# Kernel optimization log

Hardware: AMD Instinct MI355X
Metric: run time of the kernel (lower is better)

## Reference

```python
import jax, jax.numpy as jnp
import numpy as np

NEG_SLOPE = 0.2  # DGL GATConv/GATv2Conv default negative_slope


def _seg_softmax(score, dst, N):
    # softmax over incoming edges per destination node; score: (E, H)
    m = jax.ops.segment_max(score, dst, num_segments=N)          # (N, H)
    ex = jnp.exp(score - m[dst])
    s = jax.ops.segment_sum(ex, dst, num_segments=N)             # (N, H)
    return ex / s[dst]


def _gatv2(h, src, dst, Ws, Wd, attn, bias, N):
    # GATv2: e_ij = a^T LeakyReLU(W_s h_src + W_d h_dst)
    H, D = attn.shape
    fs = (h @ Ws).reshape(N, H, D)
    fd = (h @ Wd).reshape(N, H, D)
    e = jax.nn.leaky_relu(fs[src] + fd[dst], NEG_SLOPE)          # (E, H, D)
    score = jnp.einsum('ehd,hd->eh', e, attn)                    # (E, H)
    alpha = _seg_softmax(score, dst, N)
    out = jax.ops.segment_sum(fs[src] * alpha[:, :, None], dst, num_segments=N)
    return out + bias.reshape(1, H, D)                           # (N, H, D)


def _gat(h, src, dst, W, al, ar, bias, N):
    # GAT v1: e_ij = LeakyReLU(a_l . W h_src + a_r . W h_dst)
    H, D = al.shape
    f = (h @ W).reshape(N, H, D)
    el = jnp.einsum('nhd,hd->nh', f, al)
    er = jnp.einsum('nhd,hd->nh', f, ar)
    score = jax.nn.leaky_relu(el[src] + er[dst], NEG_SLOPE)      # (E, H)
    alpha = _seg_softmax(score, dst, N)
    out = jax.ops.segment_sum(f[src] * alpha[:, :, None], dst, num_segments=N)
    return out + bias.reshape(1, H, D)                           # (N, H, D)


def setup_inputs() -> dict:
    key = jax.random.key(0)
    N, E, V, ED = 50000, 800000, 32, 128   # nodes, edges, node types, embed_dim
    H, D = 4, 32                           # heads, per-head dim (hidden = 128)
    ks = jax.random.split(key, 20)
    rn = lambda k, shp, s: jax.random.normal(k, shp, dtype=jnp.float32) * s
    hid = H * D
    return {
        'in_feat': jax.random.randint(ks[0], (N,), 0, V),
        'src': jax.random.randint(ks[1], (E,), 0, N),
        'dst': jax.random.randint(ks[2], (E,), 0, N),
        'emb': rn(ks[3], (V, ED), 0.02),
        'W1s': rn(ks[4], (ED, hid), 1.0 / np.sqrt(ED)),
        'W1d': rn(ks[5], (ED, hid), 1.0 / np.sqrt(ED)),
        'a1': rn(ks[6], (H, D), 1.0 / np.sqrt(D)),
        'b1': jnp.zeros((hid,), jnp.float32),
        'W2s': rn(ks[7], (hid, hid), 1.0 / np.sqrt(hid)),
        'W2d': rn(ks[8], (hid, hid), 1.0 / np.sqrt(hid)),
        'a2': rn(ks[9], (H, D), 1.0 / np.sqrt(D)),
        'b2': jnp.zeros((hid,), jnp.float32),
        'Wc': rn(ks[10], (hid, H * V), 1.0 / np.sqrt(hid)),
        'al': rn(ks[11], (H, V), 1.0 / np.sqrt(V)),
        'ar': rn(ks[12], (H, V), 1.0 / np.sqrt(V)),
        'bc': jnp.zeros((H * V,), jnp.float32),
    }


def reference(in_feat, src, dst, emb, W1s, W1d, a1, b1, W2s, W2d, a2, b2, Wc, al, ar, bc):
    N = in_feat.shape[0]
    h = emb[in_feat]                                              # (N, 128)
    h = jax.nn.elu(_gatv2(h, src, dst, W1s, W1d, a1, b1, N).reshape(N, -1))
    h = jax.nn.elu(_gatv2(h, src, dst, W2s, W2d, a2, b2, N).reshape(N, -1))
    h = _gat(h, src, dst, Wc, al, ar, bc, N)                      # (N, H, V)
    return jax.nn.softmax(h.mean(axis=1), axis=-1)                # (N, V)
```

## Files before the change

### kernel.cpp

```cpp
#include <hip/hip_runtime.h>
#include <hip/hip_bf16.h>

typedef unsigned short u16;
typedef unsigned int u32;

typedef __bf16 bf16x8 __attribute__((ext_vector_type(8)));
typedef float f32x4 __attribute__((ext_vector_type(4)));

#define NEG_SLOPE 0.2f
#define CAP 5120

__device__ __forceinline__ float bf2f(u16 u){
  union { u32 i; float f; } c; c.i = ((u32)u) << 16; return c.f;
}
__device__ __forceinline__ u16 f2bf(float f){
  __hip_bfloat16 h = __float2bfloat16(f);
  u16 u; __builtin_memcpy(&u, &h, 2); return u;
}
__device__ __forceinline__ u32 pack2(float a, float b){
  return (u32)f2bf(a) | ((u32)f2bf(b) << 16);
}
__device__ __forceinline__ float2 bfpair(u32 v){
  union { u32 i; float f; } a, b;
  a.i = v << 16; b.i = v & 0xffff0000u;
  return make_float2(a.f, b.f);
}
__device__ __forceinline__ float lrelu(float x){
  return fmaxf(x, 0.f) + NEG_SLOPE * fminf(x, 0.f);
}
__device__ __forceinline__ float eluf(float x){
  return x > 0.f ? x : (__expf(x) - 1.f);
}
__device__ __forceinline__ bf16x8 ld_frag(const uint4* p){
  uint4 u = *p;
  bf16x8 r;
  __builtin_memcpy(&r, &u, 16);
  return r;
}

__global__ void k_probe(const u16* __restrict__ w, int* __restrict__ flag){
  int t = threadIdx.x;
  int hit = 0;
  for (int i = t; i < 4096; i += 64){
    u16 v = w[i];
    int e = (v >> 7) & 0xFF;
    if (e >= 200) hit = 1;
  }
  unsigned long long b = __ballot(hit);
  if (t == 0) flag[0] = b ? 1 : 0;
}

struct Params13 {
  const void* src[13];
  int off[13];
  int n[13];
};

__global__ void k_cvt(Params13 P, const int* __restrict__ flag, float* __restrict__ dst){
  int t = blockIdx.y;
  int i = blockIdx.x*256 + threadIdx.x;
  if (i >= P.n[t]) return;
  int f = flag[0];
  float v = f ? ((const float*)P.src[t])[i] : bf2f(((const u16*)P.src[t])[i]);
  dst[P.off[t] + i] = v;
}

__global__ void k_wprep(const float* __restrict__ pr, u16* __restrict__ wp){
  int g = blockIdx.x*256 + threadIdx.x;
  if (g >= 3*16384) return;
  int m = g >> 14;
  int e = g & 16383;
  int j    = e & 7;
  int lane = (e >> 3) & 63;
  int kb   = (e >> 9) & 3;
  int nt   = (e >> 11) & 7;
  int k = kb*32 + (lane >> 4)*8 + j;
  int n = nt*16 + (lane & 15);
  const int Woff[3] = {37120, 53504, 70144};
  wp[g] = f2bf(pr[Woff[m] + k*128 + n]);
}

__global__ void k_t1prep(const float* __restrict__ Ts, u16* __restrict__ tp){
  int g = blockIdx.x*256 + threadIdx.x;
  if (g >= 16384) return;
  int j    = g & 7;
  int lane = (g >> 3) & 63;
  int kb   = (g >> 9) & 3;
  int nt   = (g >> 11) & 7;
  int k = kb*32 + (lane >> 4)*8 + j;
  int n = nt*16 + (lane & 15);
  int h = k >> 5, hp = n >> 5, v = k & 31;
  tp[g] = (h == hp) ? f2bf(Ts[v*128 + n]) : (u16)0;
}

__global__ __launch_bounds__(256) void k_bin(
    const int* __restrict__ src, const int* __restrict__ dst, const int* __restrict__ vf,
    int* __restrict__ gcnt, u32* __restrict__ bbuf, int E){
  __shared__ int lcnt[256];
  __shared__ int lloc[256];
  int t = threadIdx.x;
  lcnt[t] = 0;
  __syncthreads();
  int base = blockIdx.x*2048;
  int s[8], d[8];
  #pragma unroll
  for (int k=0;k<8;++k){
    int i = base + k*256 + t;
    if (i < E){ s[k]=src[i]; d[k]=dst[i]; atomicAdd(&lcnt[d[k]>>8], 1); }
    else s[k] = -1;
  }
  __syncthreads();
  if (lcnt[t] > 0) lloc[t] = atomicAdd(&gcnt[t], lcnt[t]);
  __syncthreads();
  #pragma unroll
  for (int k=0;k<8;++k){
    if (s[k] >= 0){
      int b = d[k]>>8;
      int pos = atomicAdd(&lloc[b], 1);
      if (pos < CAP)
        bbuf[(size_t)b*CAP + pos] = ((u32)s[k]<<13) | ((u32)vf[s[k]]<<8) | (u32)(d[k]&255);
    }
  }
}

__global__ __launch_bounds__(256) void k_bcnt(
    const u32* __restrict__ bbuf, const int* __restrict__ gcnt,
    u32* __restrict__ H, int* __restrict__ deg, int N){
  __shared__ u32 lh[8192];
  __shared__ int ldeg[256];
  int b = blockIdx.x;
  int t = threadIdx.x;
  for (int i=t;i<8192;i+=256) lh[i]=0;
  ldeg[t]=0;
  __syncthreads();
  int n = gcnt[b]; if (n > CAP) n = CAP;
  const u32* bb = bbuf + (size_t)b*CAP;
  for (int i=t;i<n;i+=256){
    u32 it = bb[i];
    int ld = it & 255, v = (it>>8)&31;
    atomicAdd(&lh[ld*32+v], 1u);
    atomicAdd(&ldeg[ld], 1);
  }
  __syncthreads();
  int node0 = b*256;
  for (int i=t;i<8192;i+=256){
    int ld = i>>5;
    if (node0+ld < N) H[(size_t)(node0+ld)*32 + (i&31)] = lh[i];
  }
  if (node0+t < N) deg[node0+t] = ldeg[t];
}

__global__ __launch_bounds__(256) void k_csort(
    const u32* __restrict__ bbuf, const int* __restrict__ gcnt,
    const int* __restrict__ rowptr, int* __restrict__ esrc, int N){
  __shared__ int cur[256];
  int b = blockIdx.x;
  int t = threadIdx.x;
  int node0 = b*256;
  cur[t] = (node0+t < N) ? rowptr[node0+t] : 0;
  __syncthreads();
  int n = gcnt[b]; if (n > CAP) n = CAP;
  const u32* bb = bbuf + (size_t)b*CAP;
  for (int i=t;i<n;i+=256){
    u32 it = bb[i];
    int ld = it & 255;
    int pos = atomicAdd(&cur[ld], 1);
    esrc[pos] = (int)(it >> 13);
  }
}

__global__ __launch_bounds__(256) void k_bsum(const int* __restrict__ deg,
                                              int* __restrict__ bsum, int N){
  __shared__ int ws[4];
  int t = threadIdx.x;
  int i = blockIdx.x*256 + t;
  int v = (i < N) ? deg[i] : 0;
  #pragma unroll
  for (int off=32; off>=1; off>>=1) v += __shfl_down(v, off);
  if ((t & 63) == 0) ws[t>>6] = v;
  __syncthreads();
  if (t == 0) bsum[blockIdx.x] = ws[0]+ws[1]+ws[2]+ws[3];
}

__global__ void k_scanb(const int* __restrict__ bsum, int* __restrict__ boff,
                        int* __restrict__ rowptr, int nb, int N){
  int l = threadIdx.x;
  int carry = 0;
  int nChunk = (nb + 63) >> 6;
  for (int c = 0; c < nChunk; ++c){
    int idx = (c << 6) + l;
    int v = (idx < nb) ? bsum[idx] : 0;
    int x = v;
    #pragma unroll
    for (int off=1; off<64; off<<=1){
      int y = __shfl_up(x, off);
      if (l >= off) x += y;
    }
    if (idx < nb) boff[idx] = carry + x - v;
    carry += __shfl(x, 63);
  }
  if (l == 0) rowptr[N] = carry;
}

__global__ __launch_bounds__(256) void k_scan2(const int* __restrict__ deg,
                                               const int* __restrict__ boff,
                                               int* __restrict__ rowptr, int N){
  __shared__ int ws[4];
  int t = threadIdx.x;
  int i = blockIdx.x*256 + t;
  int lane = t & 63, wid = t >> 6;
  int v = (i < N) ? deg[i] : 0;
  int x = v;
  #pragma unroll
  for (int off=1; off<64; off<<=1){
    int y = __shfl_up(x, off);
    if (lane >= off) x += y;
  }
  if (lane == 63) ws[wid] = x;
  __syncthreads();
  int woff = 0;
  #pragma unroll
  for (int w=0; w<4; ++w) woff += (w < wid) ? ws[w] : 0;
  int excl = boff[blockIdx.x] + woff + x - v;
  if (i < N) rowptr[i] = excl;
}

__global__ void k_tinyA(const float* __restrict__ pr,
                        float* __restrict__ Ts, float* __restrict__ Td){
  const float* emb = pr + 0;
  const float* W1s = pr + 4096;
  const float* W1d = pr + 20480;
  int g = blockIdx.x*256 + threadIdx.x;
  int v = g >> 7, j = g & 127;
  float as = 0.f, ad = 0.f;
  for (int k = 0; k < 128; ++k){
    float e = emb[v*128 + k];
    as += e * W1s[k*128 + j];
    ad += e * W1d[k*128 + j];
  }
  Ts[g] = as; Td[g] = ad;
}

__global__ void k_tinyB(const float* __restrict__ Ts, const float* __restrict__ Td,
                        const float* __restrict__ pr, float* __restrict__ S1){
  const float* a1 = pr + 36864;
  int g = blockIdx.x*256 + threadIdx.x;
  int vd = g >> 7, vs = (g >> 2) & 31, h = g & 3;
  float acc = 0.f;
  for (int dd = 0; dd < 32; ++dd){
    float x = Ts[vs*128 + h*32 + dd] + Td[vd*128 + h*32 + dd];
    acc += a1[h*32 + dd] * lrelu(x);
  }
  S1[g] = acc;
}

__global__ void k_tinyC(const float* __restrict__ S1, float* __restrict__ Ee){
  int g = blockIdx.x*256 + threadIdx.x;
  int vd = g >> 7, h = g & 3;
  float M = -INFINITY;
  #pragma unroll 8
  for (int vs = 0; vs < 32; ++vs) M = fmaxf(M, S1[vd*128 + vs*4 + h]);
  Ee[g] = __expf(S1[g] - M);
}

__global__ __launch_bounds__(256) void k_node1w(
    const u32* __restrict__ H, const int* __restrict__ vf,
    const float* __restrict__ Ee, u16* __restrict__ wnb, int N){
  int t = threadIdx.x;
  int wid = t >> 6, lane = t & 63;
  int base = blockIdx.x * 32;
  for (int dd = wid; dd < 32; dd += 4){
    int d = base + dd;
    if (d >= N) break;
    int tt = vf[d];
    float4 w4 = make_float4(0.f,0.f,0.f,0.f);
    if (lane < 32){
      float cf = (float)H[(size_t)d*32 + lane];
      const float4 e4 = *reinterpret_cast<const float4*>(Ee + tt*128 + lane*4);
      w4.x = cf*e4.x; w4.y = cf*e4.y; w4.z = cf*e4.z; w4.w = cf*e4.w;
    }
    float4 sv = w4;
    #pragma unroll
    for (int off=1; off<32; off<<=1){
      sv.x += __shfl_xor(sv.x, off);
      sv.y += __shfl_xor(sv.y, off);
      sv.z += __shfl_xor(sv.z, off);
      sv.w += __shfl_xor(sv.w, off);
    }
    if (lane < 32){
      float ix = (sv.x > 0.f) ? 1.f/sv.x : 0.f;
      float iy = (sv.y > 0.f) ? 1.f/sv.y : 0.f;
      float iz = (sv.z > 0.f) ? 1.f/sv.z : 0.f;
      float iw = (sv.w > 0.f) ? 1.f/sv.w : 0.f;
      u16* row = wnb + (size_t)d*128;
      row[      lane] = f2bf(w4.x*ix);
      row[ 32 + lane] = f2bf(w4.y*iy);
      row[ 64 + lane] = f2bf(w4.z*iz);
      row[ 96 + lane] = f2bf(w4.w*iw);
    }
  }
}

template<bool TWO>
__global__ __launch_bounds__(256) void k_mfma(
    const u32* __restrict__ Xb, const u16* __restrict__ wpS, const u16* __restrict__ wpD,
    u16* __restrict__ outS, u16* __restrict__ outD, int N){
  int t = threadIdx.x;
  int w = t >> 6, l = t & 63;
  int row0 = blockIdx.x*64 + w*16;
  int ar = row0 + (l & 15);
  int ko = l >> 4;
  const uint4* Xq = reinterpret_cast<const uint4*>(Xb);
  bf16x8 a[4];
  #pragma unroll
  for (int kb=0;kb<4;++kb){
    if (ar < N) a[kb] = ld_frag(&Xq[(size_t)ar*16 + kb*4 + ko]);
    else { uint4 z = make_uint4(0,0,0,0); __builtin_memcpy(&a[kb], &z, 16); }
  }
  const uint4* WS = reinterpret_cast<const uint4*>(wpS);
  const uint4* WD = reinterpret_cast<const uint4*>(wpD);
  int col0 = l & 15;
  int rbase = row0 + (l>>4)*4;
  #pragma unroll
  for (int nt=0; nt<8; ++nt){
    f32x4 accS = {0.f,0.f,0.f,0.f};
    f32x4 accD = {0.f,0.f,0.f,0.f};
    #pragma unroll
    for (int kb=0;kb<4;++kb){
      bf16x8 bS = ld_frag(&WS[(nt*4 + kb)*64 + l]);
      accS = __builtin_amdgcn_mfma_f32_16x16x32_bf16(a[kb], bS, accS, 0,0,0);
      if (TWO){
        bf16x8 bD = ld_frag(&WD[(nt*4 + kb)*64 + l]);
        accD = __builtin_amdgcn_mfma_f32_16x16x32_bf16(a[kb], bD, accD, 0,0,0);
      }
    }
    int col = nt*16 + col0;
    #pragma unroll
    for (int r=0;r<4;++r){
      int rr = rbase + r;
      if (rr < N){
        outS[(size_t)rr*128 + col] = f2bf(accS[r]);
        if (TWO) outD[(size_t)rr*128 + col] = f2bf(accD[r]);
      }
    }
  }
}

__global__ __launch_bounds__(256) void k_mfma1(
    const u32* __restrict__ Xb, const u16* __restrict__ tp, const float* __restrict__ pr,
    u16* __restrict__ outB, int N){
  const float* b1 = pr + 36992;
  int t = threadIdx.x;
  int w = t >> 6, l = t & 63;
  int row0 = blockIdx.x*64 + w*16;
  int ar = row0 + (l & 15);
  int ko = l >> 4;
  const uint4* Xq = reinterpret_cast<const uint4*>(Xb);
  bf16x8 a[4];
  #pragma unroll
  for (int kb=0;kb<4;++kb){
    if (ar < N) a[kb] = ld_frag(&Xq[(size_t)ar*16 + kb*4 + ko]);
    else { uint4 z = make_uint4(0,0,0,0); __builtin_memcpy(&a[kb], &z, 16); }
  }
  const uint4* WB = reinterpret_cast<const uint4*>(tp);
  int col0 = l & 15;
  int rbase = row0 + (l>>4)*4;
  #pragma unroll
  for (int nt=0; nt<8; ++nt){
    f32x4 acc = {0.f,0.f,0.f,0.f};
    #pragma unroll
    for (int kb=0;kb<4;++kb){
      bf16x8 b = ld_frag(&WB[(nt*4 + kb)*64 + l]);
      acc = __builtin_amdgcn_mfma_f32_16x16x32_bf16(a[kb], b, acc, 0,0,0);
    }
    int col = nt*16 + col0;
    float bv = b1[col];
    #pragma unroll
    for (int r=0;r<4;++r){
      int rr = rbase + r;
      if (rr < N) outB[(size_t)rr*128 + col] = f2bf(eluf(acc[r] + bv));
    }
  }
}

#define UNPACK8(pv, fv)                                              \
  { float2 _p0 = bfpair(pv.x), _p1 = bfpair(pv.y),                   \
           _p2 = bfpair(pv.z), _p3 = bfpair(pv.w);                   \
    fv[0]=_p0.x; fv[1]=_p0.y; fv[2]=_p1.x; fv[3]=_p1.y;              \
    fv[4]=_p2.x; fv[5]=_p2.y; fv[6]=_p3.x; fv[7]=_p3.y; }

__global__ __launch_bounds__(256) void k_node2f(
    const int* __restrict__ rowptr, const int* __restrict__ esrc,
    const u32* __restrict__ fsb, const u32* __restrict__ fdb,
    const float* __restrict__ pr, u32* __restrict__ hOutB, int N){
  const float* a2 = pr + 69888;
  const float* b2 = pr + 70016;
  int t = threadIdx.x;
  int wid = t >> 6, lane = t & 63;
  int q = lane & 15, g = lane >> 4;
  int d = blockIdx.x*4 + wid;
  if (d >= N) return;
  int r0 = rowptr[d], r1 = rowptr[d+1];
  const uint4* fs4 = reinterpret_cast<const uint4*>(fsb);
  float a2r[8], fdr[8];
  {
    float4 t0 = *reinterpret_cast<const float4*>(a2 + q*8);
    float4 t1 = *reinterpret_cast<const float4*>(a2 + q*8 + 4);
    a2r[0]=t0.x; a2r[1]=t0.y; a2r[2]=t0.z; a2r[3]=t0.w;
    a2r[4]=t1.x; a2r[5]=t1.y; a2r[6]=t1.z; a2r[7]=t1.w;
    uint4 pv = reinterpret_cast<const uint4*>(fdb)[(size_t)d*16 + q];
    UNPACK8(pv, fdr);
  }
  float m = -INFINITY, ssum = 0.f;
  float acc[8] = {0.f,0.f,0.f,0.f,0.f,0.f,0.f,0.f};
  int i = r0 + g;
  for (; i + 4 < r1; i += 8){
    int s1 = esrc[i], s2 = esrc[i+4];
    uint4 pv1 = fs4[(size_t)s1*16 + q];
    uint4 pv2 = fs4[(size_t)s2*16 + q];
    float f1[8], f2[8];
    UNPACK8(pv1, f1);
    UNPACK8(pv2, f2);
    float p1a = 0.f, p1b = 0.f, p2a = 0.f, p2b = 0.f;
    #pragma unroll
    for (int k=0;k<8;++k){
      float x1 = f1[k] + fdr[k];
      float x2 = f2[k] + fdr[k];
      p1a = fmaf(a2r[k], x1, p1a);
      p1b = fmaf(a2r[k], fabsf(x1), p1b);
      p2a = fmaf(a2r[k], x2, p2a);
      p2b = fmaf(a2r[k], fabsf(x2), p2b);
    }
    float p1 = fmaf(0.6f, p1a, 0.4f*p1b);
    float p2 = fmaf(0.6f, p2a, 0.4f*p2b);
    p1 += __shfl_xor(p1, 1); p1 += __shfl_xor(p1, 2);
    p2 += __shfl_xor(p2, 1); p2 += __shfl_xor(p2, 2);
    float mn = fmaxf(m, fmaxf(p1, p2));
    float cor = __expf(m - mn);
    float w1 = __expf(p1 - mn);
    float w2 = __expf(p2 - mn);
    ssum = ssum*cor + w1 + w2;
    #pragma unroll
    for (int k=0;k<8;++k) acc[k] = fmaf(acc[k], cor, fmaf(w1, f1[k], w2*f2[k]));
    m = mn;
  }
  for (; i < r1; i += 4){
    int s = esrc[i];
    uint4 pv = fs4[(size_t)s*16 + q];
    float fv[8];
    UNPACK8(pv, fv);
    float pa = 0.f, pb = 0.f;
    #pragma unroll
    for (int k=0;k<8;++k){
      float x = fv[k] + fdr[k];
      pa = fmaf(a2r[k], x, pa);
      pb = fmaf(a2r[k], fabsf(x), pb);
    }
    float p = fmaf(0.6f, pa, 0.4f*pb);
    p += __shfl_xor(p, 1); p += __shfl_xor(p, 2);
    float mn = fmaxf(m, p);
    float cor = __expf(m - mn);
    float w = __expf(p - mn);
    ssum = ssum*cor + w;
    #pragma unroll
    for (int k=0;k<8;++k) acc[k] = fmaf(acc[k], cor, w*fv[k]);
    m = mn;
  }
  #pragma unroll
  for (int off = 16; off <= 32; off <<= 1){
    float mo  = __shfl_xor(m, off);
    float sso = __shfl_xor(ssum, off);
    float ao[8];
    #pragma unroll
    for (int k=0;k<8;++k) ao[k] = __shfl_xor(acc[k], off);
    float mn = fmaxf(m, mo);
    float c1 = (m  > -1e30f) ? __expf(m  - mn) : 0.f;
    float c2 = (mo > -1e30f) ? __expf(mo - mn) : 0.f;
    ssum = ssum*c1 + sso*c2;
    #pragma unroll
    for (int k=0;k<8;++k) acc[k] = acc[k]*c1 + ao[k]*c2;
    m = mn;
  }
  if (g == 0){
    float inv = (ssum > 0.f) ? 1.f/ssum : 0.f;
    float v0 = eluf(acc[0]*inv + b2[q*8+0]), v1 = eluf(acc[1]*inv + b2[q*8+1]);
    float v2 = eluf(acc[2]*inv + b2[q*8+2]), v3 = eluf(acc[3]*inv + b2[q*8+3]);
    float v4 = eluf(acc[4]*inv + b2[q*8+4]), v5 = eluf(acc[5]*inv + b2[q*8+5]);
    float v6 = eluf(acc[6]*inv + b2[q*8+6]), v7 = eluf(acc[7]*inv + b2[q*8+7]);
    uint4 ov;
    ov.x = pack2(v0,v1); ov.y = pack2(v2,v3);
    ov.z = pack2(v4,v5); ov.w = pack2(v6,v7);
    *reinterpret_cast<uint4*>(hOutB + (size_t)d*64 + q*4) = ov;
  }
}

__global__ __launch_bounds__(256) void k_node3f(
    const int* __restrict__ rowptr, const int* __restrict__ esrc,
    const float* __restrict__ el, const float* __restrict__ er, const u32* __restrict__ fb,
    const float* __restrict__ pr, const int* __restrict__ flag,
    void* __restrict__ out, int N){
  const float* bc = pr + 86784;
  int t = threadIdx.x;
  int wid = t >> 6, lane = t & 63;
  int q = lane & 15, g = lane >> 4;
  int h = q >> 2;
  int d = blockIdx.x*4 + wid;
  if (d >= N) return;
  int r0 = rowptr[d], r1 = rowptr[d+1];
  const uint4* f4g = reinterpret_cast<const uint4*>(fb);
  float erh = er[(size_t)d*4 + h];
  float m = -INFINITY, ssum = 0.f;
  float acc[8] = {0.f,0.f,0.f,0.f,0.f,0.f,0.f,0.f};
  int i = r0 + g;
  for (; i + 4 < r1; i += 8){
    int s1 = esrc[i], s2 = esrc[i+4];
    float sc1 = lrelu(el[(size_t)s1*4 + h] + erh);
    float sc2 = lrelu(el[(size_t)s2*4 + h] + erh);
    uint4 pv1 = f4g[(size_t)s1*16 + q];
    uint4 pv2 = f4g[(size_t)s2*16 + q];
    float f1[8], f2[8];
    UNPACK8(pv1, f1);
    UNPACK8(pv2, f2);
    float mn = fmaxf(m, fmaxf(sc1, sc2));
    float cor = __expf(m - mn);
    float w1 = __expf(sc1 - mn);
    float w2 = __expf(sc2 - mn);
    ssum = ssum*cor + w1 + w2;
    #pragma unroll
    for (int k=0;k<8;++k) acc[k] = fmaf(acc[k], cor, fmaf(w1, f1[k], w2*f2[k]));
    m = mn;
  }
  for (; i < r1; i += 4){
    int s = esrc[i];
    float sc = lrelu(el[(size_t)s*4 + h] + erh);
    uint4 pv = f4g[(size_t)s*16 + q];
    float fv[8];
    UNPACK8(pv, fv);
    float mn = fmaxf(m, sc);
    float cor = __expf(m - mn);
    float w = __expf(sc - mn);
    ssum = ssum*cor + w;
    #pragma unroll
    for (int k=0;k<8;++k) acc[k] = fmaf(acc[k], cor, w*fv[k]);
    m = mn;
  }
  #pragma unroll
  for (int off = 16; off <= 32; off <<= 1){
    float mo  = __shfl_xor(m, off);
    float sso = __shfl_xor(ssum, off);
    float ao[8];
    #pragma unroll
    for (int k=0;k<8;++k) ao[k] = __shfl_xor(acc[k], off);
    float mn = fmaxf(m, mo);
    float c1 = (m  > -1e30f) ? __expf(m  - mn) : 0.f;
    float c2 = (mo > -1e30f) ? __expf(mo - mn) : 0.f;
    ssum = ssum*c1 + sso*c2;
    #pragma unroll
    for (int k=0;k<8;++k) acc[k] = acc[k]*c1 + ao[k]*c2;
    m = mn;
  }
  float inv = (ssum > 0.f) ? 1.f/ssum : 0.f;
  float v[8];
  #pragma unroll
  for (int k=0;k<8;++k) v[k] = acc[k]*inv + bc[q*8+k];
  #pragma unroll
  for (int k=0;k<8;++k){
    v[k] += __shfl_xor(v[k], 4);
    v[k] += __shfl_xor(v[k], 8);
    v[k] *= 0.25f;
  }
  float mm = fmaxf(fmaxf(fmaxf(v[0],v[1]),fmaxf(v[2],v[3])),
                   fmaxf(fmaxf(v[4],v[5]),fmaxf(v[6],v[7])));
  mm = fmaxf(mm, __shfl_xor(mm, 1));
  mm = fmaxf(mm, __shfl_xor(mm, 2));
  float ex[8]; float se = 0.f;
  #pragma unroll
  for (int k=0;k<8;++k){ ex[k] = __expf(v[k]-mm); se += ex[k]; }
  se += __shfl_xor(se, 1);
  se += __shfl_xor(se, 2);
  float rs = 1.f/se;
  if (lane < 4){
    if (flag[0]){
      float4 o0 = make_float4(ex[0]*rs, ex[1]*rs, ex[2]*rs, ex[3]*rs);
      float4 o1 = make_float4(ex[4]*rs, ex[5]*rs, ex[6]*rs, ex[7]*rs);
      *reinterpret_cast<float4*>((float*)out + (size_t)d*32 + q*8)     = o0;
      *reinterpret_cast<float4*>((float*)out + (size_t)d*32 + q*8 + 4) = o1;
    } else {
      u32* o = (u32*)out + (size_t)d*16 + q*4;
      o[0] = pack2(ex[0]*rs, ex[1]*rs);
      o[1] = pack2(ex[2]*rs, ex[3]*rs);
      o[2] = pack2(ex[4]*rs, ex[5]*rs);
      o[3] = pack2(ex[6]*rs, ex[7]*rs);
    }
  }
}

__global__ void k_el(const u32* __restrict__ fb, const float* __restrict__ pr,
                     float* __restrict__ el, float* __restrict__ er, int N){
  const float* al = pr + 86528;
  const float* ar = pr + 86656;
  int g = blockIdx.x*256 + threadIdx.x;
  if (g >= N*4) return;
  int n = g >> 2, h = g & 3;
  const uint4* f4 = reinterpret_cast<const uint4*>(fb) + (size_t)n*16 + h*4;
  float aL=0.f, aR=0.f;
  #pragma unroll
  for (int q=0;q<4;++q){
    uint4 pv = f4[q];
    float fv[8];
    UNPACK8(pv, fv);
    const float* alp = al + h*32 + q*8;
    const float* arp = ar + h*32 + q*8;
    #pragma unroll
    for (int k=0;k<8;++k){
      aL += alp[k]*fv[k];
      aR += arp[k]*fv[k];
    }
  }
  el[g] = aL; er[g] = aR;
}

extern "C" void kernel_launch(void* const* d_in, const int* in_sizes, int n_in,
                              void* d_out, int out_size, void* d_ws, size_t ws_size,
                              hipStream_t stream){
  const int* in_feat = (const int*)d_in[0];
  const int* src     = (const int*)d_in[1];
  const int* dstA    = (const int*)d_in[2];
  const int N = in_sizes[0];
  const int E = in_sizes[1];

  char* p = (char*)d_ws;
  auto alloc = [&](size_t bytes)->char*{
    char* r = p; p += (bytes + 255) & ~(size_t)255; return r;
  };
  float* big0   = (float*)alloc((size_t)N*128*4);
  float* big1   = (float*)alloc((size_t)N*128*4);
  float* big2   = (float*)alloc((size_t)N*128*4);
  int*   deg    = (int*)alloc((size_t)N*4);
  int*   rowptr = (int*)alloc((size_t)(N+1)*4);
  int*   bsum   = (int*)alloc(1024*4);
  int*   boff   = (int*)alloc(1024*4);
  int*   esrc   = (int*)alloc((size_t)E*4);
  int*   gcnt   = (int*)alloc(256*4);
  float* Ts     = (float*)alloc(4096*4);
  float* Td     = (float*)alloc(4096*4);
  float* S1     = (float*)alloc(4096*4);
  float* Ee     = (float*)alloc(4096*4);
  float* el     = (float*)alloc((size_t)N*4*4);
  float* er     = (float*)alloc((size_t)N*4*4);
  float* parena = (float*)alloc(86912*4);
  u16*   wpack  = (u16*)alloc(4*16384*2);
  int*   flag   = (int*)alloc(256);

  u32* H    = (u32*)big0;
  u32* bbuf = (u32*)big1;
  u16* tpack = wpack + 3*16384;

  k_probe<<<1,64,0,stream>>>((const u16*)d_in[4], flag);
  Params13 P;
  const int sz[13]  = {4096,16384,16384,128,128,16384,16384,128,128,16384,128,128,128};
  int off = 0;
  for (int t = 0; t < 13; ++t){
    P.src[t] = d_in[3 + t];
    P.n[t] = sz[t];
    P.off[t] = off;
    off += sz[t];
  }
  k_cvt<<<dim3(64,13),256,0,stream>>>(P, flag, parena);
  k_wprep<<<192,256,0,stream>>>(parena, wpack);

  int nbkt = (N + 255)/256;
  hipMemsetAsync(gcnt, 0, 256*4, stream);
  int gBin = (E + 2047)/2048;
  k_bin<<<gBin,256,0,stream>>>(src, dstA, in_feat, gcnt, bbuf, E);
  k_bcnt<<<nbkt,256,0,stream>>>(bbuf, gcnt, H, deg, N);
  int nb = (N + 255)/256;
  k_bsum<<<nb,256,0,stream>>>(deg, bsum, N);
  k_scanb<<<1,64,0,stream>>>(bsum, boff, rowptr, nb, N);
  k_scan2<<<nb,256,0,stream>>>(deg, boff, rowptr, N);
  k_csort<<<nbkt,256,0,stream>>>(bbuf, gcnt, rowptr, esrc, N);

  k_tinyA<<<16,256,0,stream>>>(parena, Ts, Td);
  k_tinyB<<<16,256,0,stream>>>(Ts, Td, parena, S1);
  k_tinyC<<<16,256,0,stream>>>(S1, Ee);
  k_t1prep<<<64,256,0,stream>>>(Ts, tpack);

  u16* h1b = (u16*)big2;
  u16* wnb = (u16*)big2 + (size_t)N*128;
  int gN32 = (N + 31)/32;
  k_node1w<<<gN32,256,0,stream>>>(H, in_feat, Ee, wnb, N);
  int gG = (N + 63)/64;
  k_mfma1<<<gG,256,0,stream>>>((u32*)wnb, tpack, parena, h1b, N);

  u16* fs2b = (u16*)big0;
  u16* fd2b = (u16*)big1;
  k_mfma<true><<<gG,256,0,stream>>>((u32*)h1b, wpack, wpack + 16384, fs2b, fd2b, N);

  int gN4 = (N + 3)/4;
  u32* h2b = (u32*)big2;
  k_node2f<<<gN4,256,0,stream>>>(rowptr, esrc, (u32*)fs2b, (u32*)fd2b, parena, h2b, N);

  u16* f3b = (u16*)big0;
  k_mfma<false><<<gG,256,0,stream>>>(h2b, wpack + 32768, nullptr, f3b, nullptr, N);

  int gEl = (int)(((size_t)N*4 + 255)/256);
  k_el<<<gEl,256,0,stream>>>((u32*)f3b, parena, el, er, N);

  k_node3f<<<gN4,256,0,stream>>>(rowptr, esrc, el, er, (u32*)f3b, parena, flag, d_out, N);
}
```

Before: 231.5 us.

## Precompute linear GATv2 score terms per node and drop online-softmax max tracking

The GATv2 layer-2 score is split algebraically as LeakyReLU(x) = 0.6x + 0.4|x|. The linear part a·(fs+fd) is precomputed per node in a new k_el2 kernel, so the edge loop only evaluates the |x| term. Both aggregation kernels drop the running-max rescaling of the online softmax and accumulate exp(score) directly, which removes the correction exps and simplifies the cross-lane merge. The cost is an extra kernel launch and buffers, plus overflow risk if scores grow large, since the max is no longer subtracted.

```diff
diff --git a/kernel.cpp b/kernel.cpp
--- a/kernel.cpp
+++ b/kernel.cpp
@@ -389,15 +389,44 @@
     fv[0]=_p0.x; fv[1]=_p0.y; fv[2]=_p1.x; fv[3]=_p1.y;              \
     fv[4]=_p2.x; fv[5]=_p2.y; fv[6]=_p3.x; fv[7]=_p3.y; }
 
+__global__ void k_el2(const u32* __restrict__ fsb, const u32* __restrict__ fdb,
+                      const float* __restrict__ pr,
+                      float* __restrict__ el2, float* __restrict__ er2, int N){
+  const float* a2 = pr + 69888;
+  int g = blockIdx.x*256 + threadIdx.x;
+  if (g >= N*4) return;
+  int n = g >> 2, h = g & 3;
+  const uint4* fs4 = reinterpret_cast<const uint4*>(fsb) + (size_t)n*16 + h*4;
+  const uint4* fd4 = reinterpret_cast<const uint4*>(fdb) + (size_t)n*16 + h*4;
+  float aS=0.f, aD=0.f;
+  #pragma unroll
+  for (int q=0;q<4;++q){
+    uint4 ps = fs4[q];
+    uint4 pd = fd4[q];
+    float fs[8], fd[8];
+    UNPACK8(ps, fs);
+    UNPACK8(pd, fd);
+    const float* ap = a2 + h*32 + q*8;
+    #pragma unroll
+    for (int k=0;k<8;++k){
+      aS = fmaf(ap[k], fs[k], aS);
+      aD = fmaf(ap[k], fd[k], aD);
+    }
+  }
+  el2[g] = aS; er2[g] = aD;
+}
+
 __global__ __launch_bounds__(256) void k_node2f(
     const int* __restrict__ rowptr, const int* __restrict__ esrc,
     const u32* __restrict__ fsb, const u32* __restrict__ fdb,
+    const float* __restrict__ el2, const float* __restrict__ er2,
     const float* __restrict__ pr, u32* __restrict__ hOutB, int N){
   const float* a2 = pr + 69888;
   const float* b2 = pr + 70016;
   int t = threadIdx.x;
   int wid = t >> 6, lane = t & 63;
   int q = lane & 15, g = lane >> 4;
+  int hh = q >> 2;
   int d = blockIdx.x*4 + wid;
   if (d >= N) return;
   int r0 = rowptr[d], r1 = rowptr[d+1];
@@ -411,75 +440,53 @@
     uint4 pv = reinterpret_cast<const uint4*>(fdb)[(size_t)d*16 + q];
     UNPACK8(pv, fdr);
   }
-  float m = -INFINITY, ssum = 0.f;
+  float er2d = er2[(size_t)d*4 + hh];
+  float ssum = 0.f;
   float acc[8] = {0.f,0.f,0.f,0.f,0.f,0.f,0.f,0.f};
   int i = r0 + g;
   for (; i + 4 < r1; i += 8){
     int s1 = esrc[i], s2 = esrc[i+4];
     uint4 pv1 = fs4[(size_t)s1*16 + q];
     uint4 pv2 = fs4[(size_t)s2*16 + q];
+    float pl1 = el2[(size_t)s1*4 + hh] + er2d;
+    float pl2 = el2[(size_t)s2*4 + hh] + er2d;
     float f1[8], f2[8];
     UNPACK8(pv1, f1);
     UNPACK8(pv2, f2);
-    float p1a = 0.f, p1b = 0.f, p2a = 0.f, p2b = 0.f;
+    float pb1 = 0.f, pb2 = 0.f;
     #pragma unroll
     for (int k=0;k<8;++k){
-      float x1 = f1[k] + fdr[k];
-      float x2 = f2[k] + fdr[k];
-      p1a = fmaf(a2r[k], x1, p1a);
-      p1b = fmaf(a2r[k], fabsf(x1), p1b);
-      p2a = fmaf(a2r[k], x2, p2a);
-      p2b = fmaf(a2r[k], fabsf(x2), p2b);
-    }
-    float p1 = fmaf(0.6f, p1a, 0.4f*p1b);
-    float p2 = fmaf(0.6f, p2a, 0.4f*p2b);
-    p1 += __shfl_xor(p1, 1); p1 += __shfl_xor(p1, 2);
-    p2 += __shfl_xor(p2, 1); p2 += __shfl_xor(p2, 2);
-    float mn = fmaxf(m, fmaxf(p1, p2));
-    float cor = __expf(m - mn);
-    float w1 = __expf(p1 - mn);
-    float w2 = __expf(p2 - mn);
-    ssum = ssum*cor + w1 + w2;
-    #pragma unroll
-    for (int k=0;k<8;++k) acc[k] = fmaf(acc[k], cor, fmaf(w1, f1[k], w2*f2[k]));
-    m = mn;
+      pb1 = fmaf(a2r[k], fabsf(f1[k] + fdr[k]), pb1);
+      pb2 = fmaf(a2r[k], fabsf(f2[k] + fdr[k]), pb2);
+    }
+    pb1 += __shfl_xor(pb1, 1); pb1 += __shfl_xor(pb1, 2);
+    pb2 += __shfl_xor(pb2, 1); pb2 += __shfl_xor(pb2, 2);
+    float w1 = __expf(fmaf(0.6f, pl1, 0.4f*pb1));
+    float w2 = __expf(fmaf(0.6f, pl2, 0.4f*pb2));
+    ssum += w1 + w2;
+    #pragma unroll
+    for (int k=0;k<8;++k) acc[k] = fmaf(w1, f1[k], fmaf(w2, f2[k], acc[k]));
   }
   for (; i < r1; i += 4){
     int s = esrc[i];
     uint4 pv = fs4[(size_t)s*16 + q];
+    float pl = el2[(size_t)s*4 + hh] + er2d;
     float fv[8];
     UNPACK8(pv, fv);
-    float pa = 0.f, pb = 0.f;
-    #pragma unroll
-    for (int k=0;k<8;++k){
-      float x = fv[k] + fdr[k];
-      pa = fmaf(a2r[k], x, pa);
-      pb = fmaf(a2r[k], fabsf(x), pb);
-    }
-    float p = fmaf(0.6f, pa, 0.4f*pb);
-    p += __shfl_xor(p, 1); p += __shfl_xor(p, 2);
-    float mn = fmaxf(m, p);
-    float cor = __expf(m - mn);
-    float w = __expf(p - mn);
-    ssum = ssum*cor + w;
-    #pragma unroll
-    for (int k=0;k<8;++k) acc[k] = fmaf(acc[k], cor, w*fv[k]);
-    m = mn;
+    float pb = 0.f;
+    #pragma unroll
+    for (int k=0;k<8;++k) pb = fmaf(a2r[k], fabsf(fv[k] + fdr[k]), pb);
+    pb += __shfl_xor(pb, 1); pb += __shfl_xor(pb, 2);
+    float w = __expf(fmaf(0.6f, pl, 0.4f*pb));
+    ssum += w;
+    #pragma unroll
+    for (int k=0;k<8;++k) acc[k] = fmaf(w, fv[k], acc[k]);
   }
   #pragma unroll
   for (int off = 16; off <= 32; off <<= 1){
-    float mo  = __shfl_xor(m, off);
-    float sso = __shfl_xor(ssum, off);
-    float ao[8];
-    #pragma unroll
-    for (int k=0;k<8;++k) ao[k] = __shfl_xor(acc[k], off);
-    float mn = fmaxf(m, mo);
-    float c1 = (m  > -1e30f) ? __expf(m  - mn) : 0.f;
-    float c2 = (mo > -1e30f) ? __expf(mo - mn) : 0.f;
-    ssum = ssum*c1 + sso*c2;
-    #pragma unroll
-    for (int k=0;k<8;++k) acc[k] = acc[k]*c1 + ao[k]*c2;
-    m = mn;
+    ssum += __shfl_xor(ssum, off);
+    #pragma unroll
+    for (int k=0;k<8;++k) acc[k] += __shfl_xor(acc[k], off);
   }
   if (g == 0){
     float inv = (ssum > 0.f) ? 1.f/ssum : 0.f;
@@ -509,55 +516,37 @@
   int r0 = rowptr[d], r1 = rowptr[d+1];
   const uint4* f4g = reinterpret_cast<const uint4*>(fb);
   float erh = er[(size_t)d*4 + h];
-  float m = -INFINITY, ssum = 0.f;
+  float ssum = 0.f;
   float acc[8] = {0.f,0.f,0.f,0.f,0.f,0.f,0.f,0.f};
   int i = r0 + g;
   for (; i + 4 < r1; i += 8){
     int s1 = esrc[i], s2 = esrc[i+4];
-    float sc1 = lrelu(el[(size_t)s1*4 + h] + erh);
-    float sc2 = lrelu(el[(size_t)s2*4 + h] + erh);
+    float w1 = __expf(lrelu(el[(size_t)s1*4 + h] + erh));
+    float w2 = __expf(lrelu(el[(size_t)s2*4 + h] + erh));
     uint4 pv1 = f4g[(size_t)s1*16 + q];
     uint4 pv2 = f4g[(size_t)s2*16 + q];
     float f1[8], f2[8];
     UNPACK8(pv1, f1);
     UNPACK8(pv2, f2);
-    float mn = fmaxf(m, fmaxf(sc1, sc2));
-    float cor = __expf(m - mn);
-    float w1 = __expf(sc1 - mn);
-    float w2 = __expf(sc2 - mn);
-    ssum = ssum*cor + w1 + w2;
-    #pragma unroll
-    for (int k=0;k<8;++k) acc[k] = fmaf(acc[k], cor, fmaf(w1, f1[k], w2*f2[k]));
-    m = mn;
+    ssum += w1 + w2;
+    #pragma unroll
+    for (int k=0;k<8;++k) acc[k] = fmaf(w1, f1[k], fmaf(w2, f2[k], acc[k]));
   }
   for (; i < r1; i += 4){
     int s = esrc[i];
-    float sc = lrelu(el[(size_t)s*4 + h] + erh);
+    float w = __expf(lrelu(el[(size_t)s*4 + h] + erh));
     uint4 pv = f4g[(size_t)s*16 + q];
     float fv[8];
     UNPACK8(pv, fv);
-    float mn = fmaxf(m, sc);
-    float cor = __expf(m - mn);
-    float w = __expf(sc - mn);
-    ssum = ssum*cor + w;
-    #pragma unroll
-    for (int k=0;k<8;++k) acc[k] = fmaf(acc[k], cor, w*fv[k]);
-    m = mn;
+    ssum += w;
+    #pragma unroll
+    for (int k=0;k<8;++k) acc[k] = fmaf(w, fv[k], acc[k]);
   }
   #pragma unroll
   for (int off = 16; off <= 32; off <<= 1){
-    float mo  = __shfl_xor(m, off);
-    float sso = __shfl_xor(ssum, off);
-    float ao[8];
-    #pragma unroll
-    for (int k=0;k<8;++k) ao[k] = __shfl_xor(acc[k], off);
-    float mn = fmaxf(m, mo);
-    float c1 = (m  > -1e30f) ? __expf(m  - mn) : 0.f;
-    float c2 = (mo > -1e30f) ? __expf(mo - mn) : 0.f;
-    ssum = ssum*c1 + sso*c2;
-    #pragma unroll
-    for (int k=0;k<8;++k) acc[k] = acc[k]*c1 + ao[k]*c2;
-    m = mn;
+    ssum += __shfl_xor(ssum, off);
+    #pragma unroll
+    for (int k=0;k<8;++k) acc[k] += __shfl_xor(acc[k], off);
   }
   float inv = (ssum > 0.f) ? 1.f/ssum : 0.f;
   float v[8];
@@ -648,6 +637,8 @@
   float* Ee     = (float*)alloc(4096*4);
   float* el     = (float*)alloc((size_t)N*4*4);
   float* er     = (float*)alloc((size_t)N*4*4);
+  float* el2    = (float*)alloc((size_t)N*4*4);
+  float* er2    = (float*)alloc((size_t)N*4*4);
   float* parena = (float*)alloc(86912*4);
   u16*   wpack  = (u16*)alloc(4*16384*2);
   int*   flag   = (int*)alloc(256);
@@ -696,14 +687,16 @@
   u16* fd2b = (u16*)big1;
   k_mfma<true><<<gG,256,0,stream>>>((u32*)h1b, wpack, wpack + 16384, fs2b, fd2b, N);
 
+  int gEl = (int)(((size_t)N*4 + 255)/256);
+  k_el2<<<gEl,256,0,stream>>>((u32*)fs2b, (u32*)fd2b, parena, el2, er2, N);
+
   int gN4 = (N + 3)/4;
   u32* h2b = (u32*)big2;
-  k_node2f<<<gN4,256,0,stream>>>(rowptr, esrc, (u32*)fs2b, (u32*)fd2b, parena, h2b, N);
+  k_node2f<<<gN4,256,0,stream>>>(rowptr, esrc, (u32*)fs2b, (u32*)fd2b, el2, er2, parena, h2b, N);
 
   u16* f3b = (u16*)big0;
   k_mfma<false><<<gG,256,0,stream>>>(h2b, wpack + 32768, nullptr, f3b, nullptr, N);
 
-  int gEl = (int)(((size_t)N*4 + 255)/256);
   k_el<<<gEl,256,0,stream>>>((u32*)f3b, parena, el, er, N);
 
   k_node3f<<<gN4,256,0,stream>>>(rowptr, esrc, el, er, (u32*)f3b, parena, flag, d_out, N);
```

After: 235.7 us. About the same (+1.8%).
